# Performance work log

Measured on AMD Instinct MI355X. Metric: run time of the kernel, lower is better.

The kernel has to match this reference:

```python
import jax, jax.numpy as jnp
import numpy as np

RANGE_MIN = -5.0
RANGE_MAX = 5.0
MIN_BIN_SIZE = 1e-4
MIN_SLOPE = 1e-4
N = 33554432  # 32M elements, memory-bound
K = 8         # number of bins -> params has 3*K + 1 = 25 entries


def setup_inputs() -> dict:
    key = jax.random.key(0)
    kx, kp = jax.random.split(key)
    x = jax.random.normal(kx, (N,), dtype=jnp.float32)
    params = jax.random.normal(kp, (3 * K + 1,), dtype=jnp.float32)
    return {"x": x, "params": params}


def _normalize_params(params):
    k = (params.shape[-1] - 1) // 3
    widths_unnorm = params[:k]
    heights_unnorm = params[k:2 * k]
    slopes_unnorm = params[2 * k:]
    total_size = RANGE_MAX - RANGE_MIN
    widths = jax.nn.softmax(widths_unnorm, axis=-1) * (total_size - k * MIN_BIN_SIZE) + MIN_BIN_SIZE
    heights = jax.nn.softmax(heights_unnorm, axis=-1) * (total_size - k * MIN_BIN_SIZE) + MIN_BIN_SIZE
    slopes_offset = jnp.log(jnp.exp(1.0 - MIN_SLOPE) - 1.0)
    slopes = jax.nn.softplus(slopes_unnorm + slopes_offset) + MIN_SLOPE
    x_pos = jnp.concatenate([jnp.array([0.0], dtype=params.dtype), jnp.cumsum(widths)]) + RANGE_MIN
    y_pos = jnp.concatenate([jnp.array([0.0], dtype=params.dtype), jnp.cumsum(heights)]) + RANGE_MIN
    return x_pos, y_pos, slopes


def reference(x, params):
    x_pos, y_pos, slopes = _normalize_params(params)
    below_range = x < RANGE_MIN
    above_range = x > RANGE_MAX
    slope_left, slope_right = slopes[0], slopes[-1]
    y_linear_left = (x - RANGE_MIN) * slope_left + RANGE_MIN
    y_linear_right = (x - RANGE_MAX) * slope_right + RANGE_MAX
    logdet_linear_left = jnp.log(slope_left)
    logdet_linear_right = jnp.log(slope_right)

    num_bins = x_pos.shape[-1] - 1
    bin_idx = jnp.searchsorted(x_pos[1:-1], x, side='right')
    bin_idx = jnp.clip(bin_idx, 0, num_bins - 1)
    x_k, x_k1 = x_pos[bin_idx], x_pos[bin_idx + 1]
    y_k, y_k1 = y_pos[bin_idx], y_pos[bin_idx + 1]
    slope_k, slope_k1 = slopes[bin_idx], slopes[bin_idx + 1]

    width = x_k1 - x_k
    height = y_k1 - y_k
    xi = jnp.clip((x - x_k) / width, 0.0, 1.0)
    s = height / width
    numerator = s * xi * xi + slope_k * xi * (1.0 - xi)
    denominator = s + (slope_k1 + slope_k - 2.0 * s) * xi * (1.0 - xi)
    y_spline = y_k + height * numerator / denominator

    xi_1m = 1.0 - xi
    xi_xi_1m = xi * xi_1m
    num_derivative = s * s * (slope_k1 * xi * xi + 2.0 * s * xi_xi_1m + slope_k * xi_1m * xi_1m)
    derivative = num_derivative / (denominator * denominator)
    logdet_spline = jnp.log(derivative)

    y = jnp.where(below_range, y_linear_left, jnp.where(above_range, y_linear_right, y_spline))
    logdet = jnp.where(below_range, logdet_linear_left, jnp.where(above_range, logdet_linear_right, logdet_spline))
    return (y, logdet)
```

## Files before the change

kernel.cpp:

```cpp
#include <hip/hip_runtime.h>
#include <math.h>

#define KBINS 8
#define R_MIN -5.0f
#define R_MAX 5.0f
#define MIN_BIN 1e-4f
#define MIN_SLOPE 1e-4f

typedef float v4f __attribute__((ext_vector_type(4)));


__global__ void rqs_params_kernel(const float* __restrict__ p, float* __restrict__ ws) {
    if (threadIdx.x != 0 || blockIdx.x != 0) return;
    float w[KBINS], h[KBINS], sl[KBINS + 1];
    const float scale = (R_MAX - R_MIN) - KBINS * MIN_BIN;

    float m = -1e30f;
    for (int i = 0; i < KBINS; ++i) m = fmaxf(m, p[i]);
    float sum = 0.f;
    for (int i = 0; i < KBINS; ++i) { w[i] = expf(p[i] - m); sum += w[i]; }
    for (int i = 0; i < KBINS; ++i) w[i] = w[i] / sum * scale + MIN_BIN;

    m = -1e30f;
    for (int i = 0; i < KBINS; ++i) m = fmaxf(m, p[KBINS + i]);
    sum = 0.f;
    for (int i = 0; i < KBINS; ++i) { h[i] = expf(p[KBINS + i] - m); sum += h[i]; }
    for (int i = 0; i < KBINS; ++i) h[i] = h[i] / sum * scale + MIN_BIN;

    const float off = logf(expf(1.0f - MIN_SLOPE) - 1.0f);
    for (int i = 0; i <= KBINS; ++i) {
        float z = p[2 * KBINS + i] + off;
        float sp = (z > 20.f) ? z : log1pf(expf(z));
        sl[i] = sp + MIN_SLOPE;
    }

    float xp[KBINS + 1], yp[KBINS + 1];
    xp[0] = R_MIN; yp[0] = R_MIN;
    for (int i = 0; i < KBINS; ++i) { xp[i + 1] = xp[i] + w[i]; yp[i + 1] = yp[i] + h[i]; }

    for (int i = 0; i <= KBINS; ++i) {
        ws[i] = xp[i];
        ws[9 + i] = yp[i];
        ws[18 + i] = sl[i];
    }
    for (int b = 0; b < KBINS; ++b) {
        float width  = xp[b + 1] - xp[b];
        float height = yp[b + 1] - yp[b];
        float s = height / width;
        float* q = ws + 28 + b * 8;
        q[0] = xp[b];
        q[1] = 1.0f / width;
        q[2] = yp[b];
        q[3] = height;
        q[4] = s;
        q[5] = sl[b];
        q[6] = sl[b + 1];
        q[7] = sl[b] + sl[b + 1] - 2.0f * s;
    }
    ws[92] = logf(sl[0]);
    ws[93] = logf(sl[KBINS]);
}

__global__ __launch_bounds__(256) void rqs_main_kernel(
        const v4f* __restrict__ x4,
        const float*  __restrict__ ws,
        v4f* __restrict__ y4,
        v4f* __restrict__ ld4,
        int n4) {
    __shared__ __align__(16) v4f sbin[2 * KBINS];

    const int tid = threadIdx.x;
    if (tid < 2 * KBINS) sbin[tid] = ((const v4f*)(ws + 28))[tid];
    __syncthreads();

    const int i = blockIdx.x * blockDim.x + tid;
    if (i >= n4) return;

    const float e1 = ws[1], e2 = ws[2], e3 = ws[3], e4 = ws[4],
                e5 = ws[5], e6 = ws[6], e7 = ws[7];
    const float sl0 = ws[18], slK = ws[26];
    const float lsl0 = ws[92], lslK = ws[93];

    const v4f xv = x4[i];
    v4f yv, lv;

    #pragma unroll
    for (int j = 0; j < 4; ++j) {
        const float x = xv[j];
        int b = (int)(x >= e1) + (int)(x >= e2) + (int)(x >= e3) + (int)(x >= e4)
              + (int)(x >= e5) + (int)(x >= e6) + (int)(x >= e7);

        const v4f q0 = sbin[2 * b];
        const v4f q1 = sbin[2 * b + 1];

        float xi = (x - q0[0]) * q0[1];
        xi = fminf(fmaxf(xi, 0.f), 1.f);
        const float s = q1[0], sk = q1[1], sk1 = q1[2], c0 = q1[3];
        const float xi1m = 1.f - xi;
        const float xx   = xi * xi1m;
        const float xi2  = xi * xi;
        const float num  = s * xi2 + sk * xx;
        const float den  = s + c0 * xx;
        const float invd = __builtin_amdgcn_rcpf(den);
        float y = q0[2] + q0[3] * (num * invd);
        const float dnum  = (s * s) * (sk1 * xi2 + 2.f * s * xx + sk * (xi1m * xi1m));
        const float deriv = dnum * (invd * invd);
        float ld = __logf(deriv);

        const bool below = x < R_MIN;
        const bool above = x > R_MAX;
        const float yl = (x - R_MIN) * sl0 + R_MIN;
        const float yr = (x - R_MAX) * slK + R_MAX;
        y  = above ? yr  : y;
        y  = below ? yl  : y;
        ld = above ? lslK : ld;
        ld = below ? lsl0 : ld;

        yv[j] = y;
        lv[j] = ld;
    }

    y4[i]  = yv;
    ld4[i] = lv;
}

extern "C" void kernel_launch(void* const* d_in, const int* in_sizes, int n_in,
                              void* d_out, int out_size, void* d_ws, size_t ws_size,
                              hipStream_t stream) {
    const float* x = (const float*)d_in[0];
    const float* p = (const float*)d_in[1];
    float* out = (float*)d_out;
    float* ws  = (float*)d_ws;
    const int N = in_sizes[0];
    const int n4 = N / 4;

    rqs_params_kernel<<<1, 64, 0, stream>>>(p, ws);
    rqs_main_kernel<<<(n4 + 255) / 256, 256, 0, stream>>>(
        (const v4f*)x, ws, (v4f*)out, (v4f*)out + n4, n4);
}
```

Baseline: 354.9 us.

## Use persistent grid-stride loop with register prefetch of next input vector

Replaces the one-vector-per-thread launch with a fixed grid of 2048 blocks whose threads loop over the input with a grid stride. Each iteration loads the next float4 before computing the current one, so memory latency overlaps with compute. It also pays the shared-memory table setup and parameter loads once per block instead of once per 256 vectors. In exchange there is less parallelism in flight per wave and a fixed grid size that may not saturate bandwidth on this device.

```diff
diff --git a/kernel.cpp b/kernel.cpp
--- a/kernel.cpp
+++ b/kernel.cpp
@@ -61,6 +61,46 @@
     ws[93] = logf(sl[KBINS]);
 }
 
+__device__ __forceinline__ void rqs_elem(
+        float x, const v4f* __restrict__ sbin,
+        float e1, float e2, float e3, float e4, float e5, float e6, float e7,
+        float sl0, float slK, float lsl0, float lslK,
+        float& y_out, float& ld_out) {
+    int b = (int)(x >= e1) + (int)(x >= e2) + (int)(x >= e3) + (int)(x >= e4)
+          + (int)(x >= e5) + (int)(x >= e6) + (int)(x >= e7);
+
+    const v4f q0 = sbin[2 * b];
+    const v4f q1 = sbin[2 * b + 1];
+
+    float xi = (x - q0[0]) * q0[1];
+    xi = fminf(fmaxf(xi, 0.f), 1.f);
+    const float s = q1[0], sk = q1[1], sk1 = q1[2], c0 = q1[3];
+    const float xi1m = 1.f - xi;
+    const float xx   = xi * xi1m;
+    const float xi2  = xi * xi;
+    const float num  = s * xi2 + sk * xx;
+    const float den  = s + c0 * xx;
+    const float invd = __builtin_amdgcn_rcpf(den);
+    float y = q0[2] + q0[3] * (num * invd);
+    const float dnum  = (s * s) * (sk1 * xi2 + 2.f * s * xx + sk * (xi1m * xi1m));
+    const float deriv = dnum * (invd * invd);
+    float ld = __logf(deriv);
+
+    const bool below = x < R_MIN;
+    const bool above = x > R_MAX;
+    const float yl = (x - R_MIN) * sl0 + R_MIN;
+    const float yr = (x - R_MAX) * slK + R_MAX;
+    y  = above ? yr  : y;
+    y  = below ? yl  : y;
+    ld = above ? lslK : ld;
+    ld = below ? lsl0 : ld;
+
+    y_out = y;
+    ld_out = ld;
+}
+
+#define NBLK 2048
+
 __global__ __launch_bounds__(256) void rqs_main_kernel(
         const v4f* __restrict__ x4,
         const float*  __restrict__ ws,
@@ -73,55 +113,37 @@
     if (tid < 2 * KBINS) sbin[tid] = ((const v4f*)(ws + 28))[tid];
     __syncthreads();
 
-    const int i = blockIdx.x * blockDim.x + tid;
-    if (i >= n4) return;
-
     const float e1 = ws[1], e2 = ws[2], e3 = ws[3], e4 = ws[4],
                 e5 = ws[5], e6 = ws[6], e7 = ws[7];
     const float sl0 = ws[18], slK = ws[26];
     const float lsl0 = ws[92], lslK = ws[93];
 
-    const v4f xv = x4[i];
-    v4f yv, lv;
+    const int stride = gridDim.x * blockDim.x;
+    int i = blockIdx.x * blockDim.x + tid;
+    if (i >= n4) return;
 
-    #pragma unroll
-    for (int j = 0; j < 4; ++j) {
-        const float x = xv[j];
-        int b = (int)(x >= e1) + (int)(x >= e2) + (int)(x >= e3) + (int)(x >= e4)
-              + (int)(x >= e5) + (int)(x >= e6) + (int)(x >= e7);
+    v4f xv = x4[i];
+    for (;;) {
+        const int nxt = i + stride;
+        const bool has = nxt < n4;
+        v4f xnext;
+        if (has) xnext = x4[nxt];
 
-        const v4f q0 = sbin[2 * b];
-        const v4f q1 = sbin[2 * b + 1];
+        v4f yv, lv;
+        #pragma unroll
+        for (int j = 0; j < 4; ++j) {
+            float yt, lt;
+            rqs_elem(xv[j], sbin, e1, e2, e3, e4, e5, e6, e7,
+                     sl0, slK, lsl0, lslK, yt, lt);
+            yv[j] = yt; lv[j] = lt;
+        }
+        y4[i]  = yv;
+        ld4[i] = lv;
 
-        float xi = (x - q0[0]) * q0[1];
-        xi = fminf(fmaxf(xi, 0.f), 1.f);
-        const float s = q1[0], sk = q1[1], sk1 = q1[2], c0 = q1[3];
-        const float xi1m = 1.f - xi;
-        const float xx   = xi * xi1m;
-        const float xi2  = xi * xi;
-        const float num  = s * xi2 + sk * xx;
-        const float den  = s + c0 * xx;
-        const float invd = __builtin_amdgcn_rcpf(den);
-        float y = q0[2] + q0[3] * (num * invd);
-        const float dnum  = (s * s) * (sk1 * xi2 + 2.f * s * xx + sk * (xi1m * xi1m));
-        const float deriv = dnum * (invd * invd);
-        float ld = __logf(deriv);
-
-        const bool below = x < R_MIN;
-        const bool above = x > R_MAX;
-        const float yl = (x - R_MIN) * sl0 + R_MIN;
-        const float yr = (x - R_MAX) * slK + R_MAX;
-        y  = above ? yr  : y;
-        y  = below ? yl  : y;
-        ld = above ? lslK : ld;
-        ld = below ? lsl0 : ld;
-
-        yv[j] = y;
-        lv[j] = ld;
+        if (!has) break;
+        i = nxt;
+        xv = xnext;
     }
-
-    y4[i]  = yv;
-    ld4[i] = lv;
 }
 
 extern "C" void kernel_launch(void* const* d_in, const int* in_sizes, int n_in,
@@ -135,6 +157,6 @@
     const int n4 = N / 4;
 
     rqs_params_kernel<<<1, 64, 0, stream>>>(p, ws);
-    rqs_main_kernel<<<(n4 + 255) / 256, 256, 0, stream>>>(
+    rqs_main_kernel<<<NBLK, 256, 0, stream>>>(
         (const v4f*)x, ws, (v4f*)out, (v4f*)out + n4, n4);
 }
```

Result: slower. 368.0 us (+3.7%).
